# Kernel optimization log

Measured on AMD Instinct MI355X. Metric: run time of the kernel, lower is better.

The kernel has to match this reference:

```python
import jax, jax.numpy as jnp
import numpy as np


def _gcn_layer(x, W, b, row, col, num_nodes):
    # x: [N, F_in]; W: [F_in, F_out]; row/col: [E2] (with self-loops appended)
    xw = x @ W  # [N, F_out]
    ones = jnp.ones(row.shape[0], dtype=xw.dtype)
    deg = jax.ops.segment_sum(ones, col, num_segments=num_nodes)  # in-degree incl. self-loop
    dinv = jnp.where(deg > 0, jax.lax.rsqrt(deg), 0.0)
    norm = dinv[row] * dinv[col]  # [E2]
    msg = xw[row] * norm[:, None]  # gather + per-edge scale
    out = jax.ops.segment_sum(msg, col, num_segments=num_nodes)  # scatter-add to targets
    return out + b


def setup_inputs() -> dict:
    key = jax.random.key(0)
    k1, k2, k3, k4, k5 = jax.random.split(key, 5)
    N, E, F_in, F_hid = 100000, 640000, 128, 128
    x = jax.random.normal(k1, (N, F_in), dtype=jnp.float32)
    edge_index = jax.random.randint(k2, (2, E), 0, N, dtype=jnp.int64)
    # Glorot-style init like PyG GCNConv
    s1 = (6.0 / (F_in + F_hid)) ** 0.5
    W1 = jax.random.uniform(k3, (F_in, F_hid), jnp.float32, -s1, s1)
    b1 = jnp.zeros((F_hid,), jnp.float32)
    s2 = (6.0 / (F_hid + F_hid)) ** 0.5
    W2 = jax.random.uniform(k4, (F_hid, F_hid), jnp.float32, -s2, s2)
    b2 = jnp.zeros((F_hid,), jnp.float32)
    return {"x": x, "edge_index": edge_index, "W1": W1, "b1": b1, "W2": W2, "b2": b2}


def reference(x, edge_index, W1, b1, W2, b2):
    N = x.shape[0]
    # GCN adds self-loops before symmetric normalization (add_self_loops=True default)
    self_idx = jnp.arange(N, dtype=edge_index.dtype)
    row = jnp.concatenate([edge_index[0], self_idx])
    col = jnp.concatenate([edge_index[1], self_idx])
    h = _gcn_layer(x, W1, b1, row, col, N)
    h = jax.nn.relu(h)
    # dropout is identity in eval mode (training=False)
    out = _gcn_layer(h, W2, b2, row, col, N)
    return out
```

## Files before the change

### kernel.cpp

```cpp
#include <hip/hip_runtime.h>
#include <cstdint>
#include <cstddef>


typedef unsigned int u32;
typedef unsigned short u16;
typedef __attribute__((ext_vector_type(8))) short short8;
typedef __attribute__((ext_vector_type(4))) float f32x4;

__device__ __forceinline__ float bf2f(u32 lo16) {
  union { u32 u; float f; } c; c.u = lo16 << 16; return c.f;
}
__device__ __forceinline__ u32 f2bf(float f) {
  union { float f; u32 u; } c; c.f = f;
  return (c.u + 0x7fffu + ((c.u >> 16) & 1u)) >> 16;
}

__global__ __launch_bounds__(256) void zero_wt_kernel(
    const float* __restrict__ W1, const float* __restrict__ W2,
    u16* __restrict__ Wt1, u16* __restrict__ Wt2, u16* __restrict__ bufXW,
    int* __restrict__ cnt, int N) {
  int gt = blockIdx.x * 256 + threadIdx.x;
  if (gt < N) cnt[gt] = 0;
  if (gt < 32768) {
    const float* W = (gt < 16384) ? W1 : W2;
    u16* Wt = (gt < 16384) ? Wt1 : Wt2;
    int idx = gt & 16383;
    Wt[(idx & 127) * 128 + (idx >> 7)] = (u16)f2bf(W[idx]);
  }
  if (gt < 16) ((uint4*)(bufXW + (size_t)N * 128))[gt] = make_uint4(0, 0, 0, 0);
}

__global__ __launch_bounds__(256) void count_kernel(
    const int* __restrict__ cols, const int* __restrict__ rows,
    int* __restrict__ cnt, int E, int N) {
  int e = blockIdx.x * 256 + threadIdx.x;
  if (e >= E) return;
  int c = cols[e];
  int r = rows[e];
  if ((unsigned)c >= (unsigned)N || (unsigned)r >= (unsigned)N) return;
  atomicAdd(&cnt[c], 1);
}

__global__ __launch_bounds__(256) void scan1_kernel(
    const int* __restrict__ cnt, int* __restrict__ rowptr,
    int* __restrict__ bsum, float* __restrict__ dinv, int N) {
  __shared__ int sd[256];
  int t = threadIdx.x;
  int base = blockIdx.x * 1024 + t * 4;
  int c0 = (base + 0 < N) ? cnt[base + 0] : 0;
  int c1 = (base + 1 < N) ? cnt[base + 1] : 0;
  int c2 = (base + 2 < N) ? cnt[base + 2] : 0;
  int c3 = (base + 3 < N) ? cnt[base + 3] : 0;
  if (base + 0 < N) dinv[base + 0] = rsqrtf((float)c0 + 1.0f);
  if (base + 1 < N) dinv[base + 1] = rsqrtf((float)c1 + 1.0f);
  if (base + 2 < N) dinv[base + 2] = rsqrtf((float)c2 + 1.0f);
  if (base + 3 < N) dinv[base + 3] = rsqrtf((float)c3 + 1.0f);
  int s = c0 + c1 + c2 + c3;
  sd[t] = s;
  __syncthreads();
  for (int off = 1; off < 256; off <<= 1) {
    int v = (t >= off) ? sd[t - off] : 0;
    __syncthreads();
    sd[t] += v;
    __syncthreads();
  }
  int excl = sd[t] - s;
  if (base + 0 < N) rowptr[base + 0] = excl;
  if (base + 1 < N) rowptr[base + 1] = excl + c0;
  if (base + 2 < N) rowptr[base + 2] = excl + c0 + c1;
  if (base + 3 < N) rowptr[base + 3] = excl + c0 + c1 + c2;
  if (t == 255) bsum[blockIdx.x] = sd[255];
}

__global__ __launch_bounds__(128) void scan2_kernel(
    const int* __restrict__ bsum, int* __restrict__ bsum2,
    int* __restrict__ rowptr, int NB, int N) {
  __shared__ int sd[128];
  int t = threadIdx.x;
  int v = (t < NB) ? bsum[t] : 0;
  sd[t] = v;
  __syncthreads();
  for (int off = 1; off < 128; off <<= 1) {
    int u = (t >= off) ? sd[t - off] : 0;
    __syncthreads();
    sd[t] += u;
    __syncthreads();
  }
  bsum2[t] = sd[t] - v;
  if (t == NB - 1) rowptr[N] = sd[t];
}

__global__ __launch_bounds__(256) void scan3_kernel(
    int* __restrict__ rowptr, const int* __restrict__ bsum2, int N) {
  int t = threadIdx.x;
  int b = blockIdx.x;
  int base = b * 1024 + t * 4;
  int add = bsum2[b];
#pragma unroll
  for (int k = 0; k < 4; k++)
    if (base + k < N) rowptr[base + k] += add;
}

__global__ __launch_bounds__(256) void fill_kernel(
    const int* __restrict__ cols, const int* __restrict__ rows,
    const int* __restrict__ rowptr, int* __restrict__ cnt,
    int* __restrict__ adj, int E, int N) {
  int e = blockIdx.x * 256 + threadIdx.x;
  if (e >= E) return;
  int c = cols[e];
  int r = rows[e];
  if ((unsigned)c >= (unsigned)N || (unsigned)r >= (unsigned)N) return;
  int pos = atomicSub(&cnt[c], 1) - 1;
  if (pos >= 0) adj[rowptr[c] + pos] = r;
}

template <int A_BF16>
__global__ __launch_bounds__(256) void gemm_mfma_kernel(
    const void* __restrict__ Av, const u16* __restrict__ Wt,
    const float* __restrict__ dinv, u16* __restrict__ C, int M) {
  __shared__ u16 Ws[128][136];
  __shared__ float dv_s[128];
  const int tid = threadIdx.x;
  const int row0 = blockIdx.x * 128;

  {
    const uint4* src = (const uint4*)Wt;
#pragma unroll
    for (int i = 0; i < 8; i++) {
      int linear = tid + i * 256;
      int n = linear >> 4;
      int kq = linear & 15;
      *(uint4*)&Ws[n][kq * 8] = src[linear];
    }
  }
  if (tid < 128) {
    int gr = row0 + tid;
    dv_s[tid] = (gr < M) ? dinv[gr] : 0.f;
  }
  __syncthreads();

  const int wave = tid >> 6;
  const int lane = tid & 63;
  const int lm = lane & 15;
  const int quad = lane >> 4;
  const int m0 = wave * 32;

  f32x4 acc[2][8];
#pragma unroll
  for (int mt = 0; mt < 2; mt++)
#pragma unroll
    for (int nt = 0; nt < 8; nt++) acc[mt][nt] = (f32x4){0.f, 0.f, 0.f, 0.f};

#pragma unroll
  for (int k0 = 0; k0 < 128; k0 += 32) {
    short8 bfrag[8];
#pragma unroll
    for (int nt = 0; nt < 8; nt++)
      bfrag[nt] = *(const short8*)&Ws[nt * 16 + lm][k0 + quad * 8];

    short8 afrag[2];
#pragma unroll
    for (int mt = 0; mt < 2; mt++) {
      int gr = row0 + m0 + mt * 16 + lm;
      short8 f = (short8){0, 0, 0, 0, 0, 0, 0, 0};
      if (gr < M) {
        if (A_BF16) {
          f = *(const short8*)((const u16*)Av + (size_t)gr * 128 + k0 + quad * 8);
        } else {
          const float* Af = (const float*)Av + (size_t)gr * 128 + k0 + quad * 8;
          float4 v0 = *(const float4*)Af;
          float4 v1 = *(const float4*)(Af + 4);
          f[0] = (short)f2bf(v0.x); f[1] = (short)f2bf(v0.y);
          f[2] = (short)f2bf(v0.z); f[3] = (short)f2bf(v0.w);
          f[4] = (short)f2bf(v1.x); f[5] = (short)f2bf(v1.y);
          f[6] = (short)f2bf(v1.z); f[7] = (short)f2bf(v1.w);
        }
      }
      afrag[mt] = f;
    }

#pragma unroll
    for (int mt = 0; mt < 2; mt++)
#pragma unroll
      for (int nt = 0; nt < 8; nt++)
        acc[mt][nt] = __builtin_amdgcn_mfma_f32_16x16x32_bf16(
            afrag[mt], bfrag[nt], acc[mt][nt], 0, 0, 0);
  }

  __syncthreads();
#pragma unroll
  for (int mt = 0; mt < 2; mt++) {
    int rbase = m0 + mt * 16 + quad * 4;
#pragma unroll
    for (int r = 0; r < 4; r++) {
      int lrow = rbase + r;
      float dv = dv_s[lrow];
#pragma unroll
      for (int nt = 0; nt < 8; nt++)
        Ws[lrow][nt * 16 + lm] = (u16)f2bf(acc[mt][nt][r] * dv);
    }
  }
  __syncthreads();
#pragma unroll
  for (int i = 0; i < 8; i++) {
    int linear = tid + i * 256;
    int row = linear >> 4;
    int c8 = linear & 15;
    int grow = row0 + row;
    if (grow < M)
      *(uint4*)(C + (size_t)grow * 128 + c8 * 8) = *(const uint4*)&Ws[row][c8 * 8];
  }
}

template <int RELU, int OUT_BF16>
__global__ __launch_bounds__(256) void aggregate_kernel(
    const uint4* __restrict__ xws, const int* __restrict__ rowptr,
    const int* __restrict__ adj, const float* __restrict__ dinv,
    const float* __restrict__ bias, void* __restrict__ out, int N) {
  int node = blockIdx.x * 16 + (threadIdx.x >> 4);
  if (node >= N) return;
  int lane = threadIdx.x & 15;

  int beg = rowptr[node];
  int end = rowptr[node + 1];
  float di = dinv[node];
  float4 b0 = ((const float4*)bias)[lane * 2];
  float4 b1 = ((const float4*)bias)[lane * 2 + 1];

  float a[8];
  {
    uint4 sv = xws[(size_t)node * 16 + lane];
    a[0] = bf2f(sv.x & 0xffff); a[1] = bf2f(sv.x >> 16);
    a[2] = bf2f(sv.y & 0xffff); a[3] = bf2f(sv.y >> 16);
    a[4] = bf2f(sv.z & 0xffff); a[5] = bf2f(sv.z >> 16);
    a[6] = bf2f(sv.w & 0xffff); a[7] = bf2f(sv.w >> 16);
  }

  for (int j = beg; j < end; j += 8) {
    int sidx[8];
#pragma unroll
    for (int k = 0; k < 8; k++) {
      int jj = j + k;
      sidx[k] = (jj < end) ? adj[jj] : N;
    }
    uint4 v[8];
#pragma unroll
    for (int k = 0; k < 8; k++) v[k] = xws[(size_t)sidx[k] * 16 + lane];
#pragma unroll
    for (int k = 0; k < 8; k++) {
      a[0] += bf2f(v[k].x & 0xffff); a[1] += bf2f(v[k].x >> 16);
      a[2] += bf2f(v[k].y & 0xffff); a[3] += bf2f(v[k].y >> 16);
      a[4] += bf2f(v[k].z & 0xffff); a[5] += bf2f(v[k].z >> 16);
      a[6] += bf2f(v[k].w & 0xffff); a[7] += bf2f(v[k].w >> 16);
    }
  }

  float o[8];
  o[0] = fmaf(di, a[0], b0.x); o[1] = fmaf(di, a[1], b0.y);
  o[2] = fmaf(di, a[2], b0.z); o[3] = fmaf(di, a[3], b0.w);
  o[4] = fmaf(di, a[4], b1.x); o[5] = fmaf(di, a[5], b1.y);
  o[6] = fmaf(di, a[6], b1.z); o[7] = fmaf(di, a[7], b1.w);
  if (RELU) {
#pragma unroll
    for (int k = 0; k < 8; k++) o[k] = fmaxf(o[k], 0.f);
  }
  if (OUT_BF16) {
    uint4 p;
    p.x = f2bf(o[0]) | (f2bf(o[1]) << 16);
    p.y = f2bf(o[2]) | (f2bf(o[3]) << 16);
    p.z = f2bf(o[4]) | (f2bf(o[5]) << 16);
    p.w = f2bf(o[6]) | (f2bf(o[7]) << 16);
    ((uint4*)out)[(size_t)node * 16 + lane] = p;
  } else {
    float4* op = (float4*)out + (size_t)node * 32 + lane * 2;
    op[0] = make_float4(o[0], o[1], o[2], o[3]);
    op[1] = make_float4(o[4], o[5], o[6], o[7]);
  }
}

extern "C" void kernel_launch(void* const* d_in, const int* in_sizes, int n_in,
                              void* d_out, int out_size, void* d_ws, size_t ws_size,
                              hipStream_t stream) {
  const float* x  = (const float*)d_in[0];
  const int*   ei = (const int*)d_in[1];
  const float* W1 = (const float*)d_in[2];
  const float* b1 = (const float*)d_in[3];
  const float* W2 = (const float*)d_in[4];
  const float* b2 = (const float*)d_in[5];
  float* out = (float*)d_out;

  const int F = 128;
  const int N = in_sizes[0] / F;
  const int E = in_sizes[1] / 2;
  const int* rows = ei;
  const int* cols = ei + E;

  u16*   Wt1    = (u16*)d_ws;
  u16*   Wt2    = Wt1 + 128 * 128;
  u16*   bufXW  = Wt2 + 128 * 128;
  u16*   bufH   = bufXW + (size_t)(N + 1) * F;
  float* dinv   = (float*)(bufH + (size_t)(N + 1) * F);
  int*   cnt    = (int*)(dinv + N);
  int*   rowptr = cnt + N;
  int*   adj    = rowptr + (N + 1);
  int*   bsum   = adj + E;
  int*   bsum2  = bsum + 128;

  const int NB = (N + 1023) / 1024;
  int eblocks = (E + 255) / 256;
  int nblocks = (N + 255) / 256;

  zero_wt_kernel<<<nblocks, 256, 0, stream>>>(W1, W2, Wt1, Wt2, bufXW, cnt, N);
  count_kernel<<<eblocks, 256, 0, stream>>>(cols, rows, cnt, E, N);
  scan1_kernel<<<NB, 256, 0, stream>>>(cnt, rowptr, bsum, dinv, N);
  scan2_kernel<<<1, 128, 0, stream>>>(bsum, bsum2, rowptr, NB, N);
  scan3_kernel<<<NB, 256, 0, stream>>>(rowptr, bsum2, N);
  fill_kernel<<<eblocks, 256, 0, stream>>>(cols, rows, rowptr, cnt, adj, E, N);

  int gblocks = (N + 127) / 128;
  int ablocks = (N + 15) / 16;
  gemm_mfma_kernel<0><<<gblocks, 256, 0, stream>>>(x, Wt1, dinv, bufXW, N);
  aggregate_kernel<1, 1><<<ablocks, 256, 0, stream>>>(
      (const uint4*)bufXW, rowptr, adj, dinv, b1, bufH, N);
  gemm_mfma_kernel<1><<<gblocks, 256, 0, stream>>>(bufH, Wt2, dinv, bufXW, N);
  aggregate_kernel<0, 0><<<ablocks, 256, 0, stream>>>(
      (const uint4*)bufXW, rowptr, adj, dinv, b2, out, N);
}
```

Before: 264.2 us.

## Reorder GCN to aggregate-then-transform and fuse aggregation with MFMA GEMM

Uses the identity A(XW)=(AX)W to aggregate the dinv-prescaled inputs first, then multiplies the aggregated 64-row tile by W inside the same kernel. Bias, ReLU and the next layer's dinv prescale go into the GEMM epilogue. This removes the separate GEMM kernels and the round trip of the XW intermediate through global memory. The x-to-bf16 prescale is folded into the scan finalize kernel. In exchange each block now holds both W and the gathered tile in LDS, which may lower occupancy for the latency-bound gather phase.

After: 260.2 us. About the same (-1.5%).

```diff
diff --git a/kernel.cpp b/kernel.cpp
--- a/kernel.cpp
+++ b/kernel.cpp
@@ -18,7 +18,8 @@
 
 __global__ __launch_bounds__(256) void zero_wt_kernel(
     const float* __restrict__ W1, const float* __restrict__ W2,
-    u16* __restrict__ Wt1, u16* __restrict__ Wt2, u16* __restrict__ bufXW,
+    u16* __restrict__ Wt1, u16* __restrict__ Wt2,
+    u16* __restrict__ s1, u16* __restrict__ hp,
     int* __restrict__ cnt, int N) {
   int gt = blockIdx.x * 256 + threadIdx.x;
   if (gt < N) cnt[gt] = 0;
@@ -28,7 +29,10 @@
     int idx = gt & 16383;
     Wt[(idx & 127) * 128 + (idx >> 7)] = (u16)f2bf(W[idx]);
   }
-  if (gt < 16) ((uint4*)(bufXW + (size_t)N * 128))[gt] = make_uint4(0, 0, 0, 0);
+  if (gt < 16) {
+    ((uint4*)(s1 + (size_t)N * 128))[gt] = make_uint4(0, 0, 0, 0);
+    ((uint4*)(hp + (size_t)N * 128))[gt] = make_uint4(0, 0, 0, 0);
+  }
 }
 
 __global__ __launch_bounds__(256) void count_kernel(
@@ -91,15 +95,32 @@
   if (t == NB - 1) rowptr[N] = sd[t];
 }
 
-__global__ __launch_bounds__(256) void scan3_kernel(
-    int* __restrict__ rowptr, const int* __restrict__ bsum2, int N) {
-  int t = threadIdx.x;
-  int b = blockIdx.x;
-  int base = b * 1024 + t * 4;
-  int add = bsum2[b];
-#pragma unroll
-  for (int k = 0; k < 4; k++)
-    if (base + k < N) rowptr[base + k] += add;
+__global__ __launch_bounds__(256) void finalize_kernel(
+    const float* __restrict__ x, const float* __restrict__ dinv,
+    int* __restrict__ rowptr, const int* __restrict__ bsum2,
+    u16* __restrict__ s1, int N, int NB) {
+  int b = blockIdx.x, t = threadIdx.x;
+  if (b < NB) {
+    int base = b * 1024 + t * 4;
+    int add = bsum2[b];
+#pragma unroll
+    for (int k = 0; k < 4; k++)
+      if (base + k < N) rowptr[base + k] += add;
+  }
+  int total = N * 16;
+  for (int idx = b * 256 + t; idx < total; idx += gridDim.x * 256) {
+    int node = idx >> 4, l = idx & 15;
+    float di = dinv[node];
+    const float* xp = x + (size_t)node * 128 + l * 8;
+    float4 v0 = *(const float4*)xp;
+    float4 v1 = *(const float4*)(xp + 4);
+    uint4 p;
+    p.x = f2bf(di * v0.x) | (f2bf(di * v0.y) << 16);
+    p.y = f2bf(di * v0.z) | (f2bf(di * v0.w) << 16);
+    p.z = f2bf(di * v1.x) | (f2bf(di * v1.y) << 16);
+    p.w = f2bf(di * v1.z) | (f2bf(di * v1.w) << 16);
+    ((uint4*)s1)[idx] = p;
+  }
 }
 
 __global__ __launch_bounds__(256) void fill_kernel(
@@ -115,167 +136,136 @@
   if (pos >= 0) adj[rowptr[c] + pos] = r;
 }
 
-template <int A_BF16>
-__global__ __launch_bounds__(256) void gemm_mfma_kernel(
-    const void* __restrict__ Av, const u16* __restrict__ Wt,
-    const float* __restrict__ dinv, u16* __restrict__ C, int M) {
-  __shared__ u16 Ws[128][136];
-  __shared__ float dv_s[128];
+template <int LAYER>
+__global__ __launch_bounds__(256) void fused_ag_kernel(
+    const uint4* __restrict__ src, const int* __restrict__ rowptr,
+    const int* __restrict__ adj, const float* __restrict__ dinv,
+    const float* __restrict__ bias, const uint4* __restrict__ Wt,
+    void* __restrict__ out, int N) {
+  __shared__ __align__(16) u16 smem[128 * 136 + 64 * 136];
+  __shared__ float dv_s[64];
+  u16 (*Ws)[136] = (u16(*)[136])smem;
+  u16 (*Gs)[136] = (u16(*)[136])(smem + 128 * 136);
   const int tid = threadIdx.x;
-  const int row0 = blockIdx.x * 128;
-
-  {
-    const uint4* src = (const uint4*)Wt;
-#pragma unroll
-    for (int i = 0; i < 8; i++) {
-      int linear = tid + i * 256;
-      int n = linear >> 4;
-      int kq = linear & 15;
-      *(uint4*)&Ws[n][kq * 8] = src[linear];
-    }
-  }
-  if (tid < 128) {
-    int gr = row0 + tid;
-    dv_s[tid] = (gr < M) ? dinv[gr] : 0.f;
-  }
-  __syncthreads();
-
-  const int wave = tid >> 6;
-  const int lane = tid & 63;
-  const int lm = lane & 15;
-  const int quad = lane >> 4;
-  const int m0 = wave * 32;
-
-  f32x4 acc[2][8];
-#pragma unroll
-  for (int mt = 0; mt < 2; mt++)
-#pragma unroll
-    for (int nt = 0; nt < 8; nt++) acc[mt][nt] = (f32x4){0.f, 0.f, 0.f, 0.f};
-
-#pragma unroll
-  for (int k0 = 0; k0 < 128; k0 += 32) {
-    short8 bfrag[8];
-#pragma unroll
-    for (int nt = 0; nt < 8; nt++)
-      bfrag[nt] = *(const short8*)&Ws[nt * 16 + lm][k0 + quad * 8];
-
-    short8 afrag[2];
-#pragma unroll
-    for (int mt = 0; mt < 2; mt++) {
-      int gr = row0 + m0 + mt * 16 + lm;
-      short8 f = (short8){0, 0, 0, 0, 0, 0, 0, 0};
-      if (gr < M) {
-        if (A_BF16) {
-          f = *(const short8*)((const u16*)Av + (size_t)gr * 128 + k0 + quad * 8);
-        } else {
-          const float* Af = (const float*)Av + (size_t)gr * 128 + k0 + quad * 8;
-          float4 v0 = *(const float4*)Af;
-          float4 v1 = *(const float4*)(Af + 4);
-          f[0] = (short)f2bf(v0.x); f[1] = (short)f2bf(v0.y);
-          f[2] = (short)f2bf(v0.z); f[3] = (short)f2bf(v0.w);
-          f[4] = (short)f2bf(v1.x); f[5] = (short)f2bf(v1.y);
-          f[6] = (short)f2bf(v1.z); f[7] = (short)f2bf(v1.w);
+  const int row0 = blockIdx.x * 64;
+
+#pragma unroll
+  for (int i = 0; i < 8; i++) {
+    int linear = tid + i * 256;
+    int n = linear >> 4, kq = linear & 15;
+    *(uint4*)&Ws[n][kq * 8] = Wt[linear];
+  }
+
+  const int qw = tid >> 4;
+  const int l = tid & 15;
+#pragma unroll
+  for (int pass = 0; pass < 4; ++pass) {
+    int lrow = pass * 16 + qw;
+    int node = row0 + lrow;
+    float a[8] = {0.f, 0.f, 0.f, 0.f, 0.f, 0.f, 0.f, 0.f};
+    float di = 0.f;
+    if (node < N) {
+      di = dinv[node];
+      uint4 sv = src[(size_t)node * 16 + l];
+      a[0] = bf2f(sv.x & 0xffff); a[1] = bf2f(sv.x >> 16);
+      a[2] = bf2f(sv.y & 0xffff); a[3] = bf2f(sv.y >> 16);
+      a[4] = bf2f(sv.z & 0xffff); a[5] = bf2f(sv.z >> 16);
+      a[6] = bf2f(sv.w & 0xffff); a[7] = bf2f(sv.w >> 16);
+      int beg = rowptr[node], end = rowptr[node + 1];
+      for (int j = beg; j < end; j += 8) {
+        int sidx[8];
+#pragma unroll
+        for (int k = 0; k < 8; k++) {
+          int jj = j + k;
+          sidx[k] = (jj < end) ? adj[jj] : N;
+        }
+        uint4 v[8];
+#pragma unroll
+        for (int k = 0; k < 8; k++) v[k] = src[(size_t)sidx[k] * 16 + l];
+#pragma unroll
+        for (int k = 0; k < 8; k++) {
+          a[0] += bf2f(v[k].x & 0xffff); a[1] += bf2f(v[k].x >> 16);
+          a[2] += bf2f(v[k].y & 0xffff); a[3] += bf2f(v[k].y >> 16);
+          a[4] += bf2f(v[k].z & 0xffff); a[5] += bf2f(v[k].z >> 16);
+          a[6] += bf2f(v[k].w & 0xffff); a[7] += bf2f(v[k].w >> 16);
         }
       }
-      afrag[mt] = f;
-    }
-
-#pragma unroll
-    for (int mt = 0; mt < 2; mt++)
-#pragma unroll
-      for (int nt = 0; nt < 8; nt++)
-        acc[mt][nt] = __builtin_amdgcn_mfma_f32_16x16x32_bf16(
-            afrag[mt], bfrag[nt], acc[mt][nt], 0, 0, 0);
-  }
-
+    }
+    uint4 p;
+    p.x = f2bf(di * a[0]) | (f2bf(di * a[1]) << 16);
+    p.y = f2bf(di * a[2]) | (f2bf(di * a[3]) << 16);
+    p.z = f2bf(di * a[4]) | (f2bf(di * a[5]) << 16);
+    p.w = f2bf(di * a[6]) | (f2bf(di * a[7]) << 16);
+    *(uint4*)&Gs[lrow][l * 8] = p;
+    if (l == 0) dv_s[lrow] = di;
+  }
   __syncthreads();
-#pragma unroll
-  for (int mt = 0; mt < 2; mt++) {
-    int rbase = m0 + mt * 16 + quad * 4;
+
+  const int wave = tid >> 6, lane = tid & 63;
+  const int lm = lane & 15, quad = lane >> 4;
+  const int m0 = wave * 16;
+  f32x4 acc[8];
+#pragma unroll
+  for (int nt = 0; nt < 8; nt++) acc[nt] = (f32x4){0.f, 0.f, 0.f, 0.f};
+#pragma unroll
+  for (int k0 = 0; k0 < 128; k0 += 32) {
+    short8 afrag = *(const short8*)&Gs[m0 + lm][k0 + quad * 8];
+#pragma unroll
+    for (int nt = 0; nt < 8; nt++) {
+      short8 bfrag = *(const short8*)&Ws[nt * 16 + lm][k0 + quad * 8];
+      acc[nt] = __builtin_amdgcn_mfma_f32_16x16x32_bf16(afrag, bfrag, acc[nt], 0, 0, 0);
+    }
+  }
+
+  float bv[8];
+#pragma unroll
+  for (int nt = 0; nt < 8; nt++) bv[nt] = bias[nt * 16 + lm];
+
+  __syncthreads();
+  if (LAYER == 1) {
+    int rbase = m0 + quad * 4;
 #pragma unroll
     for (int r = 0; r < 4; r++) {
       int lrow = rbase + r;
       float dv = dv_s[lrow];
 #pragma unroll
+      for (int nt = 0; nt < 8; nt++) {
+        float v = fmaxf(acc[nt][r] + bv[nt], 0.f);
+        Gs[lrow][nt * 16 + lm] = (u16)f2bf(v * dv);
+      }
+    }
+    __syncthreads();
+    u16* C = (u16*)out;
+#pragma unroll
+    for (int i = 0; i < 4; i++) {
+      int linear = tid + i * 256;
+      int row = linear >> 4, c8 = linear & 15;
+      int grow = row0 + row;
+      if (grow < N)
+        *(uint4*)(C + (size_t)grow * 128 + c8 * 8) = *(const uint4*)&Gs[row][c8 * 8];
+    }
+  } else {
+    float (*Fs)[132] = (float(*)[132])smem;
+    int rbase = m0 + quad * 4;
+#pragma unroll
+    for (int r = 0; r < 4; r++) {
+      int lrow = rbase + r;
+#pragma unroll
       for (int nt = 0; nt < 8; nt++)
-        Ws[lrow][nt * 16 + lm] = (u16)f2bf(acc[mt][nt][r] * dv);
-    }
-  }
-  __syncthreads();
-#pragma unroll
-  for (int i = 0; i < 8; i++) {
-    int linear = tid + i * 256;
-    int row = linear >> 4;
-    int c8 = linear & 15;
-    int grow = row0 + row;
-    if (grow < M)
-      *(uint4*)(C + (size_t)grow * 128 + c8 * 8) = *(const uint4*)&Ws[row][c8 * 8];
-  }
-}
-
-template <int RELU, int OUT_BF16>
-__global__ __launch_bounds__(256) void aggregate_kernel(
-    const uint4* __restrict__ xws, const int* __restrict__ rowptr,
-    const int* __restrict__ adj, const float* __restrict__ dinv,
-    const float* __restrict__ bias, void* __restrict__ out, int N) {
-  int node = blockIdx.x * 16 + (threadIdx.x >> 4);
-  if (node >= N) return;
-  int lane = threadIdx.x & 15;
-
-  int beg = rowptr[node];
-  int end = rowptr[node + 1];
-  float di = dinv[node];
-  float4 b0 = ((const float4*)bias)[lane * 2];
-  float4 b1 = ((const float4*)bias)[lane * 2 + 1];
-
-  float a[8];
-  {
-    uint4 sv = xws[(size_t)node * 16 + lane];
-    a[0] = bf2f(sv.x & 0xffff); a[1] = bf2f(sv.x >> 16);
-    a[2] = bf2f(sv.y & 0xffff); a[3] = bf2f(sv.y >> 16);
-    a[4] = bf2f(sv.z & 0xffff); a[5] = bf2f(sv.z >> 16);
-    a[6] = bf2f(sv.w & 0xffff); a[7] = bf2f(sv.w >> 16);
-  }
-
-  for (int j = beg; j < end; j += 8) {
-    int sidx[8];
-#pragma unroll
-    for (int k = 0; k < 8; k++) {
-      int jj = j + k;
-      sidx[k] = (jj < end) ? adj[jj] : N;
-    }
-    uint4 v[8];
-#pragma unroll
-    for (int k = 0; k < 8; k++) v[k] = xws[(size_t)sidx[k] * 16 + lane];
-#pragma unroll
-    for (int k = 0; k < 8; k++) {
-      a[0] += bf2f(v[k].x & 0xffff); a[1] += bf2f(v[k].x >> 16);
-      a[2] += bf2f(v[k].y & 0xffff); a[3] += bf2f(v[k].y >> 16);
-      a[4] += bf2f(v[k].z & 0xffff); a[5] += bf2f(v[k].z >> 16);
-      a[6] += bf2f(v[k].w & 0xffff); a[7] += bf2f(v[k].w >> 16);
-    }
-  }
-
-  float o[8];
-  o[0] = fmaf(di, a[0], b0.x); o[1] = fmaf(di, a[1], b0.y);
-  o[2] = fmaf(di, a[2], b0.z); o[3] = fmaf(di, a[3], b0.w);
-  o[4] = fmaf(di, a[4], b1.x); o[5] = fmaf(di, a[5], b1.y);
-  o[6] = fmaf(di, a[6], b1.z); o[7] = fmaf(di, a[7], b1.w);
-  if (RELU) {
-#pragma unroll
-    for (int k = 0; k < 8; k++) o[k] = fmaxf(o[k], 0.f);
-  }
-  if (OUT_BF16) {
-    uint4 p;
-    p.x = f2bf(o[0]) | (f2bf(o[1]) << 16);
-    p.y = f2bf(o[2]) | (f2bf(o[3]) << 16);
-    p.z = f2bf(o[4]) | (f2bf(o[5]) << 16);
-    p.w = f2bf(o[6]) | (f2bf(o[7]) << 16);
-    ((uint4*)out)[(size_t)node * 16 + lane] = p;
-  } else {
-    float4* op = (float4*)out + (size_t)node * 32 + lane * 2;
-    op[0] = make_float4(o[0], o[1], o[2], o[3]);
-    op[1] = make_float4(o[4], o[5], o[6], o[7]);
+        Fs[lrow][nt * 16 + lm] = acc[nt][r] + bv[nt];
+    }
+    __syncthreads();
+    float* C = (float*)out;
+#pragma unroll
+    for (int i = 0; i < 8; i++) {
+      int linear = tid + i * 256;
+      int row = linear >> 5, c4 = linear & 31;
+      int grow = row0 + row;
+      if (grow < N) {
+        f32x4 v = *(const f32x4*)&Fs[row][c4 * 4];
+        __builtin_nontemporal_store(v, (f32x4*)(C + (size_t)grow * 128 + c4 * 4));
+      }
+    }
   }
 }
 
@@ -298,9 +288,9 @@
 
   u16*   Wt1    = (u16*)d_ws;
   u16*   Wt2    = Wt1 + 128 * 128;
-  u16*   bufXW  = Wt2 + 128 * 128;
-  u16*   bufH   = bufXW + (size_t)(N + 1) * F;
-  float* dinv   = (float*)(bufH + (size_t)(N + 1) * F);
+  u16*   s1     = Wt2 + 128 * 128;
+  u16*   hp     = s1 + (size_t)(N + 1) * F;
+  float* dinv   = (float*)(hp + (size_t)(N + 1) * F);
   int*   cnt    = (int*)(dinv + N);
   int*   rowptr = cnt + N;
   int*   adj    = rowptr + (N + 1);
@@ -310,20 +300,18 @@
   const int NB = (N + 1023) / 1024;
   int eblocks = (E + 255) / 256;
   int nblocks = (N + 255) / 256;
-
-  zero_wt_kernel<<<nblocks, 256, 0, stream>>>(W1, W2, Wt1, Wt2, bufXW, cnt, N);
+  int fblocks = (NB > 784) ? NB : 784;
+
+  zero_wt_kernel<<<nblocks, 256, 0, stream>>>(W1, W2, Wt1, Wt2, s1, hp, cnt, N);
   count_kernel<<<eblocks, 256, 0, stream>>>(cols, rows, cnt, E, N);
   scan1_kernel<<<NB, 256, 0, stream>>>(cnt, rowptr, bsum, dinv, N);
   scan2_kernel<<<1, 128, 0, stream>>>(bsum, bsum2, rowptr, NB, N);
-  scan3_kernel<<<NB, 256, 0, stream>>>(rowptr, bsum2, N);
+  finalize_kernel<<<fblocks, 256, 0, stream>>>(x, dinv, rowptr, bsum2, s1, N, NB);
   fill_kernel<<<eblocks, 256, 0, stream>>>(cols, rows, rowptr, cnt, adj, E, N);
 
-  int gblocks = (N + 127) / 128;
-  int ablocks = (N + 15) / 16;
-  gemm_mfma_kernel<0><<<gblocks, 256, 0, stream>>>(x, Wt1, dinv, bufXW, N);
-  aggregate_kernel<1, 1><<<ablocks, 256, 0, stream>>>(
-      (const uint4*)bufXW, rowptr, adj, dinv, b1, bufH, N);
-  gemm_mfma_kernel<1><<<gblocks, 256, 0, stream>>>(bufH, Wt2, dinv, bufXW, N);
-  aggregate_kernel<0, 0><<<ablocks, 256, 0, stream>>>(
-      (const uint4*)bufXW, rowptr, adj, dinv, b2, out, N);
-}
+  int gblocks = (N + 63) / 64;
+  fused_ag_kernel<1><<<gblocks, 256, 0, stream>>>(
+      (const uint4*)s1, rowptr, adj, dinv, b1, (const uint4*)Wt1, hp, N);
+  fused_ag_kernel<2><<<gblocks, 256, 0, stream>>>(
+      (const uint4*)hp, rowptr, adj, dinv, b2, (const uint4*)Wt2, out, N);
+}
```
